# Performance work log

Measured on AMD Instinct MI355X. Metric: run time of the kernel, lower is better.

## Reference

```python
import jax, jax.numpy as jnp
import numpy as np

N = 32768          # n_atoms
E = 524288         # n_edges (avg degree 16)
MUL = 8            # multiplicity of 0e and 1o in irreps_in/out
NB = 8             # n_basis
HR = 64            # hidden_radial
NTP = 4 * MUL * MUL  # tensor-product weight_numel (4 CG paths)
AVG_NEI = 16.0
INV_SQRT3 = 1.0 / np.sqrt(3.0)      # w3j(1,1,0) component
ALPHA = 1.0 / np.sqrt(2.0 * MUL)    # path normalization: fan_in = 2 paths * mul_in*mul_sh


def setup_inputs() -> dict:
    key = jax.random.key(0)
    ks = jax.random.split(key, 12)
    h = jax.random.normal(ks[0], (N, 4 * MUL), jnp.float32)            # [N, 8 scalars + 8*3 vectors]
    edge_index = jax.random.randint(ks[1], (2, E), 0, N)               # [2, E] int
    edge_sh = jax.random.normal(ks[2], (E, 4), jnp.float32)            # [E, 1x0e + 1x1o]
    edge_radial = jax.random.uniform(ks[3], (E, NB), jnp.float32)      # [E, n_basis]

    def lin(k, fi, fo):
        return (jax.random.normal(k, (fi, fo), jnp.float32) / np.sqrt(fi)).astype(jnp.float32)

    W1 = lin(ks[4], NB, HR); b1 = jnp.zeros((HR,), jnp.float32)
    W2 = lin(ks[5], HR, HR); b2 = jnp.zeros((HR,), jnp.float32)
    W3 = lin(ks[6], HR, NTP); b3 = jnp.zeros((NTP,), jnp.float32)
    Ws = jax.random.normal(ks[7], (MUL, MUL), jnp.float32)             # self-interaction, scalar block
    Wv = jax.random.normal(ks[8], (MUL, MUL), jnp.float32)             # self-interaction, vector block
    return dict(h=h, edge_index=edge_index, edge_sh=edge_sh, edge_radial=edge_radial,
                n_atoms=N, W1=W1, b1=b1, W2=W2, b2=b2, W3=W3, b3=b3, Ws=Ws, Wv=Wv)


def reference(h, edge_index, edge_sh, edge_radial, n_atoms, W1, b1, W2, b2, W3, b3, Ws, Wv):
    src, dst = edge_index[0], edge_index[1]

    # radial MLP -> per-edge tensor-product weights [E, 256]
    x = jax.nn.silu(edge_radial @ W1 + b1)
    x = jax.nn.silu(x @ W2 + b2)
    tpw = x @ W3 + b3
    P = MUL * MUL
    W00  = tpw[:, 0 * P:1 * P].reshape(-1, MUL, MUL)  # 0e x 0e -> 0e
    W110 = tpw[:, 1 * P:2 * P].reshape(-1, MUL, MUL)  # 1o x 1o -> 0e (dot)
    W01  = tpw[:, 2 * P:3 * P].reshape(-1, MUL, MUL)  # 0e x 1o -> 1o
    W10  = tpw[:, 3 * P:4 * P].reshape(-1, MUL, MUL)  # 1o x 0e -> 1o

    hs = h[:, :MUL]                         # [N, 8] scalars
    hv = h[:, MUL:].reshape(-1, MUL, 3)     # [N, 8, 3] vectors
    hs_e = hs[src]                          # gather [E, 8]
    hv_e = hv[src]                          # gather [E, 8, 3]
    sh0 = edge_sh[:, 0]                     # [E]
    sh1 = edge_sh[:, 1:4]                   # [E, 3]

    # equivariant tensor product (e3nn FullyConnectedTensorProduct, l<=1)
    m0 = ALPHA * (jnp.einsum('eu,euw->ew', hs_e * sh0[:, None], W00)
                  + INV_SQRT3 * jnp.einsum('eui,ei,euw->ew', hv_e, sh1, W110))       # [E, 8]
    m1 = ALPHA * (jnp.einsum('eu,ei,euw->ewi', hs_e, sh1, W01)
                  + jnp.einsum('eui,euw->ewi', hv_e * sh0[:, None, None], W10))      # [E, 8, 3]
    messages = jnp.concatenate([m0, m1.reshape(-1, 3 * MUL)], axis=-1)               # [E, 32]

    # scatter-add to destination nodes, degree normalization
    agg = jax.ops.segment_sum(messages, dst, num_segments=n_atoms) / np.sqrt(AVG_NEI)

    # self interaction (o3.Linear: block-diagonal per irrep, 1/sqrt(fan_in))
    self0 = (hs @ Ws) / np.sqrt(MUL)
    self1 = jnp.einsum('nui,uw->nwi', hv, Wv) / np.sqrt(MUL)
    h_self = jnp.concatenate([self0, self1.reshape(-1, 3 * MUL)], axis=-1)

    return h_self + agg
```

## Files before the change

kernel.cpp:

```cpp
#include <hip/hip_runtime.h>

#define N_ATOMS 32768
#define E_EDGES 524288
#define FEAT 32
#define TPB 512
#define WPB 8
#define PASSES 2
#define GRID (E_EDGES / (WPB * PASSES * 16))
#define INV_SQRT3 0.57735026919f
#define MSG_SCALE 0.0625f
#define SELF_SCALE 0.35355339059f

#define WS_MSG   0
#define WS_CNT   33554432
#define WS_CUR   33685504
#define WS_OFFS  33816576
#define WS_BSUM  33947648
#define WS_BBASE 33948160
#define WS_WF    36045824

typedef _Float16 f16;
typedef __attribute__((ext_vector_type(8))) _Float16 f16x8;
typedef __attribute__((ext_vector_type(4))) float f32x4;
typedef __attribute__((ext_vector_type(2))) _Float16 f16x2;
typedef __attribute__((ext_vector_type(4))) _Float16 f16x4;

__device__ __forceinline__ float silu(float x) { return x / (1.0f + __expf(-x)); }

__device__ __forceinline__ f32x4 mfma16(f16x8 a, f16x8 b, f32x4 c) {
    return __builtin_amdgcn_mfma_f32_16x16x32_f16(a, b, c, 0, 0, 0);
}

__global__ __launch_bounds__(256) void prep_kernel(
    const float* __restrict__ W1, const float* __restrict__ W2,
    const float* __restrict__ W3, f16* __restrict__ wf)
{
    int idx = blockIdx.x * 256 + threadIdx.x;
    float v;
    if (idx < 2048) {
        int f = idx;
        int n0 = f >> 9, lane = (f >> 3) & 63, j = f & 7;
        int k = ((lane >> 4) << 3) + j, n = (n0 << 4) + (lane & 15);
        v = (k < 8) ? W1[k * 64 + n] : 0.0f;
    } else if (idx < 6144) {
        int f = idx - 2048;
        int kk = f >> 11, n0 = (f >> 9) & 3, lane = (f >> 3) & 63, j = f & 7;
        int k = (kk << 5) + ((lane >> 4) << 3) + j, n = (n0 << 4) + (lane & 15);
        v = W2[k * 64 + n];
    } else {
        int f = idx - 6144;
        int kk = f >> 13, n0 = (f >> 9) & 15, lane = (f >> 3) & 63, j = f & 7;
        int k = (kk << 5) + ((lane >> 4) << 3) + j, n = (n0 << 4) + (lane & 15);
        v = W3[k * 256 + n];
    }
    wf[idx] = (f16)v;
}

__global__ __launch_bounds__(256) void count_kernel(const int* __restrict__ eidx,
                                                    int* __restrict__ cnt) {
    int e = blockIdx.x * 256 + threadIdx.x;
    atomicAdd(&cnt[eidx[E_EDGES + e]], 1);
}

__global__ __launch_bounds__(256) void scan1_kernel(const int* __restrict__ cnt,
                                                    int* __restrict__ bsum) {
    __shared__ int s[256];
    int t = threadIdx.x;
    s[t] = cnt[blockIdx.x * 256 + t];
    __syncthreads();
    for (int d = 128; d > 0; d >>= 1) {
        if (t < d) s[t] += s[t + d];
        __syncthreads();
    }
    if (t == 0) bsum[blockIdx.x] = s[0];
}

__global__ __launch_bounds__(64) void scan2_kernel(const int* __restrict__ bsum,
                                                   int* __restrict__ bbase) {
    int lane = threadIdx.x;
    int v0 = bsum[2 * lane], v1 = bsum[2 * lane + 1];
    int s = v0 + v1, x = s;
    for (int d = 1; d < 64; d <<= 1) {
        int y = __shfl_up(x, d, 64);
        if (lane >= d) x += y;
    }
    int excl = x - s;
    bbase[2 * lane] = excl;
    bbase[2 * lane + 1] = excl + v0;
}

__global__ __launch_bounds__(256) void scan3_kernel(const int* __restrict__ cnt,
                                                    const int* __restrict__ bbase,
                                                    int* __restrict__ offs) {
    int t = threadIdx.x, lane = t & 63, w = t >> 6;
    int v = cnt[blockIdx.x * 256 + t];
    int x = v;
    for (int d = 1; d < 64; d <<= 1) {
        int y = __shfl_up(x, d, 64);
        if (lane >= d) x += y;
    }
    __shared__ int wsum[4];
    if (lane == 63) wsum[w] = x;
    __syncthreads();
    int base = bbase[blockIdx.x];
    for (int i = 0; i < w; ++i) base += wsum[i];
    offs[blockIdx.x * 256 + t] = base + x - v;
}

__global__ __launch_bounds__(TPB, 4) void edge_kernel(
    const float* __restrict__ h, const int* __restrict__ eidx,
    const float* __restrict__ esh, const float* __restrict__ erad,
    const f16* __restrict__ wf,
    const float* __restrict__ b1, const float* __restrict__ b2,
    const float* __restrict__ b3,
    const int* __restrict__ offs, int* __restrict__ cur,
    f16* __restrict__ msg)
{
    __shared__ f16x8 w3L[2048];
    __shared__ float b1s[64], b2s[64], b3s[256];
    __shared__ __align__(16) char xtp[WPB][16 * 72 * 2];

    const int tid = threadIdx.x;
    {
        const f16x8* wfW3 = (const f16x8*)(wf + 6144);
#pragma unroll
        for (int i = 0; i < 4; ++i)
            w3L[tid + i * TPB] = wfW3[tid + i * TPB];
    }
    if (tid < 64) { b1s[tid] = b1[tid]; b2s[tid] = b2[tid]; }
    if (tid < 256) b3s[tid] = b3[tid];
    __syncthreads();

    const f16x8* w1f = (const f16x8*)(wf);
    const f16x8* w2f = (const f16x8*)(wf + 2048);

    const int wave = tid >> 6, lane = tid & 63;
    const int g = lane >> 4, m = lane & 15;
    const int me = lane >> 2, w0 = (lane & 3) * 2;

    f16* xs = (f16*)&xtp[wave][0];
    float* tpt = (float*)&xtp[wave][0];

    for (int pass = 0; pass < PASSES; ++pass) {
        const int tile = (blockIdx.x * WPB + wave) * PASSES + pass;
        const int e0 = tile * 16;

        f16x8 arad;
        {
            float r[8] = {0.f, 0.f, 0.f, 0.f, 0.f, 0.f, 0.f, 0.f};
            if (g == 0) {
                const float4* rp = (const float4*)(erad + (long)(e0 + m) * 8);
                float4 r0 = rp[0], r1 = rp[1];
                r[0] = r0.x; r[1] = r0.y; r[2] = r0.z; r[3] = r0.w;
                r[4] = r1.x; r[5] = r1.y; r[6] = r1.z; r[7] = r1.w;
            }
#pragma unroll
            for (int j = 0; j < 8; ++j) arad[j] = (f16)r[j];
        }

#pragma unroll
        for (int n0 = 0; n0 < 4; ++n0) {
            f32x4 acc = {};
            acc = mfma16(arad, w1f[n0 * 64 + lane], acc);
            float bn = b1s[n0 * 16 + m];
#pragma unroll
            for (int q = 0; q < 4; ++q) {
                float v = silu(acc[q] + bn);
                xs[(g * 4 + q) * 72 + n0 * 16 + m] = (f16)v;
            }
        }
        f16x8 a2[2];
        a2[0] = *(const f16x8*)(xs + m * 72 + g * 8);
        a2[1] = *(const f16x8*)(xs + m * 72 + 32 + g * 8);

        const int src = eidx[e0 + me];
        const int dst = eidx[E_EDGES + e0 + me];
        const float4 shv = *(const float4*)(esh + (long)(e0 + me) * 4);
        float hrow[32];
        {
            const float* hp = h + (long)src * FEAT;
#pragma unroll
            for (int c4 = 0; c4 < 8; ++c4)
                ((float4*)hrow)[c4] = ((const float4*)hp)[c4];
        }
        int rowid = 0;
        if ((lane & 3) == 0)
            rowid = offs[dst] + atomicAdd(&cur[dst], 1);
        rowid = __shfl(rowid, me * 4);

#pragma unroll
        for (int n0 = 0; n0 < 4; ++n0) {
            f32x4 acc = {};
            acc = mfma16(a2[0], w2f[n0 * 64 + lane], acc);
            acc = mfma16(a2[1], w2f[(4 + n0) * 64 + lane], acc);
            float bn = b2s[n0 * 16 + m];
#pragma unroll
            for (int q = 0; q < 4; ++q) {
                float v = silu(acc[q] + bn);
                xs[(g * 4 + q) * 72 + n0 * 16 + m] = (f16)v;
            }
        }
        f16x8 a3[2];
        a3[0] = *(const f16x8*)(xs + m * 72 + g * 8);
        a3[1] = *(const f16x8*)(xs + m * 72 + 32 + g * 8);

        float m0a0 = 0.f, m0a1 = 0.f, s20 = 0.f, s21 = 0.f;
        float sv[6] = {0.f, 0.f, 0.f, 0.f, 0.f, 0.f};

#pragma unroll
        for (int t = 0; t < 16; ++t) {
            const int c = t >> 2, n0 = t & 3;
            f32x4 acc = {};
            acc = mfma16(a3[0], w3L[(c * 4 + n0) * 64 + lane], acc);
            acc = mfma16(a3[1], w3L[(16 + c * 4 + n0) * 64 + lane], acc);
            float bn = b3s[c * 64 + n0 * 16 + m];
            float* tb = tpt + (t & 1) * 288;
#pragma unroll
            for (int q = 0; q < 4; ++q)
                tb[(g * 4 + q) * 18 + m] = acc[q] + bn;
            if (t > 0) {
                const int tp = t - 1, cp = tp >> 2, np = tp & 3;
                const float* rb = tpt + (tp & 1) * 288;
#pragma unroll
                for (int uu = 0; uu < 2; ++uu) {
                    const int u = 2 * np + uu;
                    float2 tv = *(const float2*)(rb + me * 18 + uu * 8 + w0);
                    if (cp == 0) {
                        float a0 = hrow[u] * shv.x;
                        m0a0 += a0 * tv.x; m0a1 += a0 * tv.y;
                    } else if (cp == 1) {
                        float a1 = INV_SQRT3 * (hrow[8 + u * 3] * shv.y +
                                                hrow[9 + u * 3] * shv.z +
                                                hrow[10 + u * 3] * shv.w);
                        m0a0 += a1 * tv.x; m0a1 += a1 * tv.y;
                    } else if (cp == 2) {
                        s20 += hrow[u] * tv.x; s21 += hrow[u] * tv.y;
                    } else {
                        sv[0] += hrow[8 + u * 3] * tv.x;
                        sv[1] += hrow[9 + u * 3] * tv.x;
                        sv[2] += hrow[10 + u * 3] * tv.x;
                        sv[3] += hrow[8 + u * 3] * tv.y;
                        sv[4] += hrow[9 + u * 3] * tv.y;
                        sv[5] += hrow[10 + u * 3] * tv.y;
                    }
                }
            }
        }
        {
            const float* rb = tpt + 288;
#pragma unroll
            for (int uu = 0; uu < 2; ++uu) {
                const int u = 6 + uu;
                float2 tv = *(const float2*)(rb + me * 18 + uu * 8 + w0);
                sv[0] += hrow[8 + u * 3] * tv.x;
                sv[1] += hrow[9 + u * 3] * tv.x;
                sv[2] += hrow[10 + u * 3] * tv.x;
                sv[3] += hrow[8 + u * 3] * tv.y;
                sv[4] += hrow[9 + u * 3] * tv.y;
                sv[5] += hrow[10 + u * 3] * tv.y;
            }
        }

        f16* row = msg + (long)rowid * FEAT;
        f16x2 p0;
        p0[0] = (f16)(MSG_SCALE * m0a0);
        p0[1] = (f16)(MSG_SCALE * m0a1);
        *(f16x2*)(row + w0) = p0;
        f16 m1v[6];
#pragma unroll
        for (int i = 0; i < 3; ++i) {
            float s1i = (i == 0) ? shv.y : (i == 1) ? shv.z : shv.w;
            m1v[i]     = (f16)(MSG_SCALE * (s1i * s20 + shv.x * sv[i]));
            m1v[3 + i] = (f16)(MSG_SCALE * (s1i * s21 + shv.x * sv[3 + i]));
        }
        f16* rp = row + 8 + 3 * w0;
        { f16x2 t2; t2[0] = m1v[0]; t2[1] = m1v[1]; *(f16x2*)(rp)     = t2; }
        { f16x2 t2; t2[0] = m1v[2]; t2[1] = m1v[3]; *(f16x2*)(rp + 2) = t2; }
        { f16x2 t2; t2[0] = m1v[4]; t2[1] = m1v[5]; *(f16x2*)(rp + 4) = t2; }
    }
}

__global__ __launch_bounds__(256) void gather_kernel(
    const f16* __restrict__ msg,
    const int* __restrict__ offs, const int* __restrict__ cnt,
    const float* __restrict__ h,
    const float* __restrict__ Ws, const float* __restrict__ Wv,
    float* __restrict__ out)
{
    const int t = threadIdx.x;
    const int n = blockIdx.x * 32 + (t >> 3);
    const int L = t & 7;
    const int base = offs[n], deg = cnt[n];

    float a0 = 0.f, a1 = 0.f, a2 = 0.f, a3 = 0.f;
    float c0 = 0.f, c1 = 0.f, c2 = 0.f, c3 = 0.f;
    int i = 0;
    for (; i + 1 < deg; i += 2) {
        f16x4 v = *(const f16x4*)(msg + (long)(base + i) * FEAT + L * 4);
        f16x4 w = *(const f16x4*)(msg + (long)(base + i + 1) * FEAT + L * 4);
        a0 += (float)v[0]; a1 += (float)v[1]; a2 += (float)v[2]; a3 += (float)v[3];
        c0 += (float)w[0]; c1 += (float)w[1]; c2 += (float)w[2]; c3 += (float)w[3];
    }
    if (i < deg) {
        f16x4 v = *(const f16x4*)(msg + (long)(base + i) * FEAT + L * 4);
        a0 += (float)v[0]; a1 += (float)v[1]; a2 += (float)v[2]; a3 += (float)v[3];
    }
    a0 += c0; a1 += c1; a2 += c2; a3 += c3;

    const float* hrow = h + (long)n * FEAT;
    const int f0 = L * 4;
    float o[4];
    if (L < 2) {
#pragma unroll
        for (int j = 0; j < 4; ++j) {
            int w = f0 + j;
            float a = 0.f;
#pragma unroll
            for (int u = 0; u < 8; ++u) a += hrow[u] * Ws[u * 8 + w];
            o[j] = SELF_SCALE * a;
        }
    } else {
#pragma unroll
        for (int j = 0; j < 4; ++j) {
            int f = f0 + j, w = (f - 8) / 3, i3 = (f - 8) % 3;
            float a = 0.f;
#pragma unroll
            for (int u = 0; u < 8; ++u) a += hrow[8 + u * 3 + i3] * Wv[u * 8 + w];
            o[j] = SELF_SCALE * a;
        }
    }
    float4 r;
    r.x = o[0] + a0; r.y = o[1] + a1; r.z = o[2] + a2; r.w = o[3] + a3;
    *(float4*)(out + (long)n * FEAT + f0) = r;
}

extern "C" void kernel_launch(void* const* d_in, const int* in_sizes, int n_in,
                              void* d_out, int out_size, void* d_ws, size_t ws_size,
                              hipStream_t stream)
{
    const float* h    = (const float*)d_in[0];
    const int*   eidx = (const int*)  d_in[1];
    const float* esh  = (const float*)d_in[2];
    const float* erad = (const float*)d_in[3];
    const float* W1   = (const float*)d_in[5];
    const float* b1   = (const float*)d_in[6];
    const float* W2   = (const float*)d_in[7];
    const float* b2   = (const float*)d_in[8];
    const float* W3   = (const float*)d_in[9];
    const float* b3   = (const float*)d_in[10];
    const float* Ws   = (const float*)d_in[11];
    const float* Wv   = (const float*)d_in[12];
    float* out = (float*)d_out;

    char* ws = (char*)d_ws;
    f16* msg   = (f16*)(ws + WS_MSG);
    int* cnt   = (int*)(ws + WS_CNT);
    int* cur   = (int*)(ws + WS_CUR);
    int* offs  = (int*)(ws + WS_OFFS);
    int* bsum  = (int*)(ws + WS_BSUM);
    int* bbase = (int*)(ws + WS_BBASE);
    f16* wf    = (f16*)(ws + WS_WF);

    hipMemsetAsync(cnt, 0, 2 * N_ATOMS * sizeof(int), stream);

    prep_kernel<<<88, 256, 0, stream>>>(W1, W2, W3, wf);
    count_kernel<<<E_EDGES / 256, 256, 0, stream>>>(eidx, cnt);
    scan1_kernel<<<N_ATOMS / 256, 256, 0, stream>>>(cnt, bsum);
    scan2_kernel<<<1, 64, 0, stream>>>(bsum, bbase);
    scan3_kernel<<<N_ATOMS / 256, 256, 0, stream>>>(cnt, bbase, offs);
    edge_kernel<<<GRID, TPB, 0, stream>>>(h, eidx, esh, erad, wf,
                                          b1, b2, b3, offs, cur, msg);
    gather_kernel<<<N_ATOMS / 32, 256, 0, stream>>>(msg, offs, cnt,
                                                    h, Ws, Wv, out);
}
```

Baseline: 180.7 us.

## Move edge bucketing to separate fill kernel, write messages in edge order

The per-edge atomic slot assignment moves out of the edge kernel into a new fill kernel that builds a CSR list of edge ids per destination. The edge kernel now writes messages contiguously in edge order, and the gather kernel reads through the edge-id indirection. The aim is to take atomics and scattered writes out of the heavy MLP kernel. The cost is an extra kernel and random reads in the gather. The edge kernel also changes to 1024-thread blocks with one pass per wave and a different launch bound.

```diff
diff --git a/kernel.cpp b/kernel.cpp
--- a/kernel.cpp
+++ b/kernel.cpp
@@ -3,9 +3,9 @@
 #define N_ATOMS 32768
 #define E_EDGES 524288
 #define FEAT 32
-#define TPB 512
-#define WPB 8
-#define PASSES 2
+#define TPB 1024
+#define WPB 16
+#define PASSES 1
 #define GRID (E_EDGES / (WPB * PASSES * 16))
 #define INV_SQRT3 0.57735026919f
 #define MSG_SCALE 0.0625f
@@ -17,6 +17,7 @@
 #define WS_OFFS  33816576
 #define WS_BSUM  33947648
 #define WS_BBASE 33948160
+#define WS_EIDS  33948672
 #define WS_WF    36045824
 
 typedef _Float16 f16;
@@ -107,13 +108,22 @@
     offs[blockIdx.x * 256 + t] = base + x - v;
 }
 
-__global__ __launch_bounds__(TPB, 4) void edge_kernel(
+__global__ __launch_bounds__(256) void fill_kernel(const int* __restrict__ eidx,
+                                                   const int* __restrict__ offs,
+                                                   int* __restrict__ cur,
+                                                   int* __restrict__ eids) {
+    int e = blockIdx.x * 256 + threadIdx.x;
+    int d = eidx[E_EDGES + e];
+    int slot = atomicAdd(&cur[d], 1);
+    eids[offs[d] + slot] = e;
+}
+
+__global__ __launch_bounds__(TPB, 8) void edge_kernel(
     const float* __restrict__ h, const int* __restrict__ eidx,
     const float* __restrict__ esh, const float* __restrict__ erad,
     const f16* __restrict__ wf,
     const float* __restrict__ b1, const float* __restrict__ b2,
     const float* __restrict__ b3,
-    const int* __restrict__ offs, int* __restrict__ cur,
     f16* __restrict__ msg)
 {
     __shared__ f16x8 w3L[2048];
@@ -124,7 +134,7 @@
     {
         const f16x8* wfW3 = (const f16x8*)(wf + 6144);
 #pragma unroll
-        for (int i = 0; i < 4; ++i)
+        for (int i = 0; i < 2; ++i)
             w3L[tid + i * TPB] = wfW3[tid + i * TPB];
     }
     if (tid < 64) { b1s[tid] = b1[tid]; b2s[tid] = b2[tid]; }
@@ -141,8 +151,8 @@
     f16* xs = (f16*)&xtp[wave][0];
     float* tpt = (float*)&xtp[wave][0];
 
-    for (int pass = 0; pass < PASSES; ++pass) {
-        const int tile = (blockIdx.x * WPB + wave) * PASSES + pass;
+    {
+        const int tile = blockIdx.x * WPB + wave;
         const int e0 = tile * 16;
 
         f16x8 arad;
@@ -174,7 +184,6 @@
         a2[1] = *(const f16x8*)(xs + m * 72 + 32 + g * 8);
 
         const int src = eidx[e0 + me];
-        const int dst = eidx[E_EDGES + e0 + me];
         const float4 shv = *(const float4*)(esh + (long)(e0 + me) * 4);
         float hrow[32];
         {
@@ -183,10 +192,6 @@
             for (int c4 = 0; c4 < 8; ++c4)
                 ((float4*)hrow)[c4] = ((const float4*)hp)[c4];
         }
-        int rowid = 0;
-        if ((lane & 3) == 0)
-            rowid = offs[dst] + atomicAdd(&cur[dst], 1);
-        rowid = __shfl(rowid, me * 4);
 
 #pragma unroll
         for (int n0 = 0; n0 < 4; ++n0) {
@@ -261,7 +266,7 @@
             }
         }
 
-        f16* row = msg + (long)rowid * FEAT;
+        f16* row = msg + (long)(e0 + me) * FEAT;
         f16x2 p0;
         p0[0] = (f16)(MSG_SCALE * m0a0);
         p0[1] = (f16)(MSG_SCALE * m0a1);
@@ -281,7 +286,7 @@
 }
 
 __global__ __launch_bounds__(256) void gather_kernel(
-    const f16* __restrict__ msg,
+    const f16* __restrict__ msg, const int* __restrict__ eids,
     const int* __restrict__ offs, const int* __restrict__ cnt,
     const float* __restrict__ h,
     const float* __restrict__ Ws, const float* __restrict__ Wv,
@@ -296,13 +301,15 @@
     float c0 = 0.f, c1 = 0.f, c2 = 0.f, c3 = 0.f;
     int i = 0;
     for (; i + 1 < deg; i += 2) {
-        f16x4 v = *(const f16x4*)(msg + (long)(base + i) * FEAT + L * 4);
-        f16x4 w = *(const f16x4*)(msg + (long)(base + i + 1) * FEAT + L * 4);
+        int e0 = eids[base + i], e1 = eids[base + i + 1];
+        f16x4 v = *(const f16x4*)(msg + (long)e0 * FEAT + L * 4);
+        f16x4 w = *(const f16x4*)(msg + (long)e1 * FEAT + L * 4);
         a0 += (float)v[0]; a1 += (float)v[1]; a2 += (float)v[2]; a3 += (float)v[3];
         c0 += (float)w[0]; c1 += (float)w[1]; c2 += (float)w[2]; c3 += (float)w[3];
     }
     if (i < deg) {
-        f16x4 v = *(const f16x4*)(msg + (long)(base + i) * FEAT + L * 4);
+        int e0 = eids[base + i];
+        f16x4 v = *(const f16x4*)(msg + (long)e0 * FEAT + L * 4);
         a0 += (float)v[0]; a1 += (float)v[1]; a2 += (float)v[2]; a3 += (float)v[3];
     }
     a0 += c0; a1 += c1; a2 += c2; a3 += c3;
@@ -359,6 +366,7 @@
     int* offs  = (int*)(ws + WS_OFFS);
     int* bsum  = (int*)(ws + WS_BSUM);
     int* bbase = (int*)(ws + WS_BBASE);
+    int* eids  = (int*)(ws + WS_EIDS);
     f16* wf    = (f16*)(ws + WS_WF);
 
     hipMemsetAsync(cnt, 0, 2 * N_ATOMS * sizeof(int), stream);
@@ -368,8 +376,9 @@
     scan1_kernel<<<N_ATOMS / 256, 256, 0, stream>>>(cnt, bsum);
     scan2_kernel<<<1, 64, 0, stream>>>(bsum, bbase);
     scan3_kernel<<<N_ATOMS / 256, 256, 0, stream>>>(cnt, bbase, offs);
+    fill_kernel<<<E_EDGES / 256, 256, 0, stream>>>(eidx, offs, cur, eids);
     edge_kernel<<<GRID, TPB, 0, stream>>>(h, eidx, esh, erad, wf,
-                                          b1, b2, b3, offs, cur, msg);
-    gather_kernel<<<N_ATOMS / 32, 256, 0, stream>>>(msg, offs, cnt,
+                                          b1, b2, b3, msg);
+    gather_kernel<<<N_ATOMS / 32, 256, 0, stream>>>(msg, eids, offs, cnt,
                                                     h, Ws, Wv, out);
 }
```

New measurement: 318.3 us. 1.76x slower.
